# Optimization experiments

Measured on AMD Instinct MI355X. Metric: run time of the kernel, lower is better.

## Reference

```python
import jax, jax.numpy as jnp
import numpy as np
from jax import lax

# fixed perception filters from the paper (ident, sobel_x, sobel_x^T, laplacian)
_IDENT = jnp.array([[0., 0., 0.], [0., 1., 0.], [0., 0., 0.]], dtype=jnp.float32)
_SOBEL_X = jnp.array([[-1., 0., 1.], [-2., 0., 2.], [-1., 0., 1.]], dtype=jnp.float32)
_LAP = jnp.array([[1., 2., 1.], [2., -12., 2.], [1., 2., 1.]], dtype=jnp.float32)
_FILT = jnp.stack([_IDENT, _SOBEL_X, _SOBEL_X.T, _LAP])  # [4,3,3]


def _perceive(x):
    # x: [b, c, h, w] -> [b, 4c, h, w] via circular-pad depthwise 3x3 stencils
    b, c, h, w = x.shape
    y = x.reshape(b * c, 1, h, w)
    y = jnp.pad(y, ((0, 0), (0, 0), (1, 1), (1, 1)), mode='wrap')  # circular pad
    y = lax.conv_general_dilated(y, _FILT[:, None], (1, 1), 'VALID',
                                 dimension_numbers=('NCHW', 'OIHW', 'NCHW'))
    return y.reshape(b, 4 * c, h, w)


def _conv1x1(x, w, b=None):
    # w: [O, C, 1, 1]
    y = jnp.einsum('bchw,oc->bohw', x, w[:, :, 0, 0])
    if b is not None:
        y = y + b[None, :, None, None]
    return y


def _up(z, hw):
    b, c, _, _ = z.shape
    return jax.image.resize(z, (b, c, hw[0], hw[1]), method='bilinear')


def setup_inputs() -> dict:
    key = jax.random.key(0)
    ks = jax.random.split(key, 12)
    D, B = 12, 16
    inp = {
        'x0': jax.random.uniform(ks[0], (B, D, 256, 256), dtype=jnp.float32),
        'x1': jax.random.uniform(ks[1], (B, D, 128, 128), dtype=jnp.float32),
        'x2': jax.random.uniform(ks[2], (B, D, 64, 64), dtype=jnp.float32),
        'w0_1': jax.random.normal(ks[3], (96, 96, 1, 1), dtype=jnp.float32) * 0.05,
        'b0_1': jax.random.normal(ks[4], (96,), dtype=jnp.float32) * 0.05,
        'w0_2': jax.random.normal(ks[5], (D, 96, 1, 1), dtype=jnp.float32) * 0.05,
        'w1_1': jax.random.normal(ks[6], (96, 96, 1, 1), dtype=jnp.float32) * 0.05,
        'b1_1': jax.random.normal(ks[7], (96,), dtype=jnp.float32) * 0.05,
        'w1_2': jax.random.normal(ks[8], (D, 96, 1, 1), dtype=jnp.float32) * 0.05,
        'w2_1': jax.random.normal(ks[9], (96, 48, 1, 1), dtype=jnp.float32) * 0.05,
        'b2_1': jax.random.normal(ks[10], (96,), dtype=jnp.float32) * 0.05,
        'w2_2': jax.random.normal(ks[11], (D, 96, 1, 1), dtype=jnp.float32) * 0.05,
    }
    return inp


def reference(x0, x1, x2, w0_1, b0_1, w0_2, w1_1, b1_1, w1_2, w2_1, b2_1, w2_2):
    z0 = _perceive(x0)  # [B,48,256,256]
    z1 = _perceive(x1)  # [B,48,128,128]
    z2 = _perceive(x2)  # [B,48,64,64]

    # resolution 0: concat with upsampled z1 (to img_size/1)
    h0 = jnp.concatenate([z0, _up(z1, (256, 256))], axis=1)  # [B,96,256,256]
    out0 = _conv1x1(jax.nn.relu(_conv1x1(h0, w0_1, b0_1)), w0_2)

    # resolution 1: concat with upsampled z2 (to img_size/2)
    h1 = jnp.concatenate([z1, _up(z2, (128, 128))], axis=1)  # [B,96,128,128]
    out1 = _conv1x1(jax.nn.relu(_conv1x1(h1, w1_1, b1_1)), w1_2)

    # last resolution: no concat, residual add
    out2 = _conv1x1(jax.nn.relu(_conv1x1(z2, w2_1, b2_1)), w2_2) + x2

    return (out0, out1, out2)
```

## Files before the change

kernel.cpp:

```cpp
#include <hip/hip_runtime.h>


namespace {
constexpr int NB = 16;
constexpr int ND = 12;
}

typedef __attribute__((ext_vector_type(8))) _Float16 f16x8;
typedef __attribute__((ext_vector_type(2))) __fp16  hf16x2;
typedef __attribute__((ext_vector_type(8))) short   s16x8;
typedef __attribute__((ext_vector_type(4))) short   s16x4;
typedef __attribute__((ext_vector_type(4))) float   f32x4;

__device__ __forceinline__ unsigned short f2h(float f) {
    return __builtin_bit_cast(unsigned short, (_Float16)f);
}
__device__ __forceinline__ f16x8 splat8(float x) {
    _Float16 h = (_Float16)x;
    f16x8 v = {h,h,h,h,h,h,h,h};
    return v;
}
__device__ __forceinline__ f16x8 ld8(const unsigned short* p) {
    return __builtin_bit_cast(f16x8, *(const s16x8*)p);
}
__device__ __forceinline__ void st8(unsigned short* p, f16x8 v) {
    *(s16x8*)p = __builtin_bit_cast(s16x8, v);
}

__device__ __forceinline__ void up_taps(int y, int Hc, int& y0, int& y1, float& t1) {
    int j = y >> 1;
    if (y & 1) { y0 = j;            y1 = min(j+1, Hc-1); t1 = 0.25f; }
    else       { y0 = max(j-1, 0);  y1 = j;              t1 = 0.75f; }
}

__device__ __forceinline__ s16x8 repack(f16x8 q0, f16x8 q1, f16x8 q2, f16x8 q3, int j) {
    s16x8 o;
#pragma unroll
    for (int t = 0; t < 8; ++t) {
        int cl = 2*j + (t >> 2);
        _Float16 vv = ((t&3)==0) ? q0[cl] : ((t&3)==1) ? q1[cl]
                    : ((t&3)==2) ? q2[cl] : q3[cl];
        o[t] = (short)__builtin_bit_cast(unsigned short, vv);
    }
    return o;
}

template<int H, int W>
__device__ __forceinline__ void perceive_body(const float* __restrict__ x,
                                              unsigned short* __restrict__ z,
                                              int gid, int tid,
                                              unsigned short* S) {
    constexpr int HW = H*W;
    constexpr int TPX = W/16, BPI = (H/8)*TPX;
    const int b   = gid / BPI;
    const int rem = gid - b*BPI;
    const int tx  = (rem % TPX)*16, ty = (rem / TPX)*8;

#pragma unroll
    for (int i = 0; i < 12; ++i) {
        int e = i*256 + tid;
        if (e < 2880) {
            int c = e / 180, r = e - c*180;
            int ri = r / 18, ci = r - ri*18;
            int gy = (ty - 1 + ri) & (H-1);
            int gx = (tx - 1 + ci) & (W-1);
            unsigned short v = 0;
            if (c < 12) v = f2h(x[(b*ND + c)*HW + gy*W + gx]);
            S[r*16 + c] = v;
        }
    }
    __syncthreads();

    const int p = tid >> 1, h = tid & 1;
    const int py = p >> 4, px = p & 15;
    const unsigned short* Sc = &S[(py*18 + px)*16 + 8*h];
    f16x8 n00=ld8(Sc+0),   n01=ld8(Sc+16),  n02=ld8(Sc+32);
    f16x8 n10=ld8(Sc+288), n11=ld8(Sc+304), n12=ld8(Sc+320);
    f16x8 n20=ld8(Sc+576), n21=ld8(Sc+592), n22=ld8(Sc+608);
    f16x8 two = splat8(2.f), twelve = splat8(12.f);
    f16x8 sx  = (n02-n00) + two*(n12-n10) + (n22-n20);
    f16x8 sy  = (n20-n00) + two*(n21-n01) + (n22-n02);
    f16x8 lap = ((n00+n02)+(n20+n22)) + two*((n01+n10)+(n12+n21)) - twelve*n11;
    unsigned short* zp = z + ((size_t)(b*H + ty+py)*W + tx+px)*48 + 32*h;
    const int nchunk = 4 - 2*h;
#pragma unroll
    for (int j = 0; j < 4; ++j) {
        s16x8 o = repack(n11, sx, sy, lap, j);
        if (j < nchunk) *(s16x8*)(zp + 8*j) = o;
    }
}

__global__ __launch_bounds__(256)
void prep_kernel(const float* __restrict__ x0, const float* __restrict__ x1,
                 const float* __restrict__ x2,
                 const float* __restrict__ w01, const float* __restrict__ w11,
                 const float* __restrict__ w21,
                 const float* __restrict__ w02, const float* __restrict__ w12,
                 const float* __restrict__ w22,
                 unsigned short* __restrict__ x0cl,
                 unsigned short* __restrict__ z1h, unsigned short* __restrict__ z2h,
                 unsigned short* __restrict__ w1f0, unsigned short* __restrict__ w1f1,
                 unsigned short* __restrict__ w1f2,
                 unsigned short* __restrict__ w2h0, unsigned short* __restrict__ w2h1,
                 unsigned short* __restrict__ w2h2)
{
    __shared__ unsigned short S[2880];
    const int tid = threadIdx.x;
    const int bid = blockIdx.x;
    if (bid < 110) {
        int i = bid*256 + tid;
        if (i < 28032) {
            if (i < 9216) {
                int kg = i / 768, rm = i - kg*768, n = rm >> 3, j = rm & 7;
                w1f0[i] = f2h(w01[n*96 + kg*8 + j]);
            } else if (i < 18432) {
                int e = i - 9216;
                int kg = e / 768, rm = e - kg*768, n = rm >> 3, j = rm & 7;
                w1f1[e] = f2h(w11[n*96 + kg*8 + j]);
            } else if (i < 24576) {
                int e = i - 18432;
                int kg = e / 768, rm = e - kg*768, n = rm >> 3, j = rm & 7;
                w1f2[e] = (kg < 6) ? f2h(w21[n*48 + kg*8 + j]) : (unsigned short)0;
            } else {
                int e = i - 24576;
                const float* w = (e < 1152) ? w02 : (e < 2304) ? w12 : w22;
                unsigned short* d = (e < 1152) ? w2h0 : (e < 2304) ? w2h1 : w2h2;
                int q = (e >= 2304) ? e-2304 : (e >= 1152) ? e-1152 : e;
                d[q] = f2h(w[q]);
            }
        }
    } else if (bid < 110 + 4096) {
        int pix = (bid-110)*256 + tid;
        int b = pix >> 16, rem = pix & 65535;
        const float* xp = x0 + (size_t)b*ND*65536 + rem;
        s16x8 r0, r1;
#pragma unroll
        for (int c = 0; c < 8; ++c) r0[c] = (short)f2h(xp[c*65536]);
#pragma unroll
        for (int c = 0; c < 4; ++c) r1[c] = (short)f2h(xp[(8+c)*65536]);
#pragma unroll
        for (int c = 4; c < 8; ++c) r1[c] = 0;
        unsigned short* d = &x0cl[(size_t)pix*16];
        *(s16x8*)d       = r0;
        *(s16x8*)(d + 8) = r1;
    } else if (bid < 110 + 4096 + 2048) {
        perceive_body<128,128>(x1, z1h, bid - (110+4096), tid, S);
    } else {
        perceive_body<64,64>(x2, z2h, bid - (110+4096+2048), tid, S);
    }
}

template<int RES>
__device__ __forceinline__
void res_body(const unsigned short* __restrict__ xcl,
              const unsigned short* __restrict__ zown,
              const unsigned short* __restrict__ zc,
              const float* __restrict__ xres,
              const unsigned short* __restrict__ w1f,
              const float* __restrict__ b1,
              const unsigned short* __restrict__ w2h,
              float* __restrict__ out,
              int bid, int tid, unsigned short* Alds)
{
    constexpr int H  = (RES==0)?256:(RES==1)?128:64;
    constexpr int W  = H, Hc = H/2, Wc = W/2;
    constexpr int HW = H*W;
    constexpr int TPX = W/16, BPI = (H/16)*TPX;
    constexpr int NBLK = NB*BPI;
    constexpr int NK  = (RES==2)?2:3;

    constexpr int cpx = NBLK >> 3;
    const int gid = (bid & 7)*cpx + (bid >> 3);
    const int b   = gid / BPI;
    const int rem = gid - b*BPI;
    const int tx  = (rem % TPX)*16, ty = (rem / TPX)*16;

    const int wid = tid >> 6, lane = tid & 63;
    const int fr  = lane & 15, g = lane >> 4;
    const int r   = tid;
    const int py  = r >> 4, px = r & 15;
    const int gy  = ty + py, gx = tx + px;

    if (RES == 0) {
        int ym=(gy-1)&(H-1), yp=(gy+1)&(H-1);
        int xm=(gx-1)&(W-1), xq=(gx+1)&(W-1);
        const unsigned short* bp = xcl + (size_t)b*HW*16;
        const int r00=(ym*W+xm)*16, r01=(ym*W+gx)*16, r02=(ym*W+xq)*16;
        const int r10=(gy*W+xm)*16, r11=(gy*W+gx)*16, r12=(gy*W+xq)*16;
        const int r20=(yp*W+xm)*16, r21=(yp*W+gx)*16, r22=(yp*W+xq)*16;
#pragma unroll
        for (int grp = 0; grp < 2; ++grp) {
            const int off = grp*8;
            f16x8 n00=ld8(&bp[r00+off]), n01=ld8(&bp[r01+off]), n02=ld8(&bp[r02+off]);
            f16x8 n10=ld8(&bp[r10+off]), n11=ld8(&bp[r11+off]), n12=ld8(&bp[r12+off]);
            f16x8 n20=ld8(&bp[r20+off]), n21=ld8(&bp[r21+off]), n22=ld8(&bp[r22+off]);
            f16x8 two = splat8(2.f), twelve = splat8(12.f);
            f16x8 sx  = (n02-n00) + two*(n12-n10) + (n22-n20);
            f16x8 sy  = (n20-n00) + two*(n21-n01) + (n22-n02);
            f16x8 lap = ((n00+n02)+(n20+n22)) + two*((n01+n10)+(n12+n21)) - twelve*n11;
            const int jn = grp ? 2 : 4;
#pragma unroll
            for (int j = 0; j < 4; ++j) {
                s16x8 o = repack(n11, sx, sy, lap, j);
                if (j < jn) *(s16x8*)&Alds[(grp*4 + j)*2048 + r*8] = o;
            }
        }
    } else {
        const unsigned short* src = &zown[((size_t)(b*H + gy)*W + gx)*48];
#pragma unroll
        for (int j = 0; j < 6; ++j)
            *(s16x8*)&Alds[j*2048 + r*8] = *(const s16x8*)&src[8*j];
        if (RES == 2) {
            s16x8 zz = {0,0,0,0,0,0,0,0};
            *(s16x8*)&Alds[6*2048 + r*8] = zz;
            *(s16x8*)&Alds[7*2048 + r*8] = zz;
        }
    }

    if (RES != 2) {
        int ys0, ys1, xs0, xs1; float tyw, txw;
        up_taps(gy, Hc, ys0, ys1, tyw);
        up_taps(gx, Wc, xs0, xs1, txw);
        float wy0 = 1.f - tyw, wx0 = 1.f - txw;
        f16x8 w00 = splat8(wy0*wx0), w01v = splat8(wy0*txw);
        f16x8 w10 = splat8(tyw*wx0), w11v = splat8(tyw*txw);
        const int o00 = ((b*Hc + ys0)*Wc + xs0)*48;
        const int o01 = ((b*Hc + ys0)*Wc + xs1)*48;
        const int o10 = ((b*Hc + ys1)*Wc + xs0)*48;
        const int o11 = ((b*Hc + ys1)*Wc + xs1)*48;
#pragma unroll
        for (int j = 0; j < 6; ++j) {
            f16x8 t00 = ld8(&zc[o00 + 8*j]);
            f16x8 t01 = ld8(&zc[o01 + 8*j]);
            f16x8 t10 = ld8(&zc[o10 + 8*j]);
            f16x8 t11 = ld8(&zc[o11 + 8*j]);
            f16x8 v = t00*w00 + t01*w01v + t10*w10 + t11*w11v;
            st8(&Alds[(6 + j)*2048 + r*8], v);
        }
    }

    f16x8 w1r[3][6];
#pragma unroll
    for (int ks = 0; ks < NK; ++ks)
#pragma unroll
        for (int nt = 0; nt < 6; ++nt)
            w1r[ks][nt] = ld8(&w1f[((ks*4 + g)*96 + nt*16 + fr)*8]);
    f16x8 w2r[3];
#pragma unroll
    for (int ks = 0; ks < 3; ++ks) {
        s16x8 v = {0,0,0,0,0,0,0,0};
        if (fr < 12) v = *(const s16x8*)&w2h[fr*96 + ks*32 + g*8];
        w2r[ks] = __builtin_bit_cast(f16x8, v);
    }

#pragma unroll 1
    for (int h2 = 0; h2 < 2; ++h2) {
        const int rbase = wid*64 + h2*32;

        f32x4 acc[2][6] = {};
#pragma unroll
        for (int ks = 0; ks < NK; ++ks) {
            const int kgo = (ks*4 + g)*2048;
            f16x8 a0 = ld8(&Alds[kgo + (rbase +      fr)*8]);
            f16x8 a1 = ld8(&Alds[kgo + (rbase + 16 + fr)*8]);
#pragma unroll
            for (int nt = 0; nt < 6; ++nt) {
                acc[0][nt] = __builtin_amdgcn_mfma_f32_16x16x32_f16(w1r[ks][nt], a0, acc[0][nt], 0, 0, 0);
                acc[1][nt] = __builtin_amdgcn_mfma_f32_16x16x32_f16(w1r[ks][nt], a1, acc[1][nt], 0, 0, 0);
            }
        }

#pragma unroll
        for (int nt = 0; nt < 6; ++nt) {
            const float4 bv4 = *(const float4*)&b1[nt*16 + g*4];
#pragma unroll
            for (int pt = 0; pt < 2; ++pt) {
                float h0 = fmaxf(acc[pt][nt][0] + bv4.x, 0.f);
                float h1 = fmaxf(acc[pt][nt][1] + bv4.y, 0.f);
                float h2f_ = fmaxf(acc[pt][nt][2] + bv4.z, 0.f);
                float h3 = fmaxf(acc[pt][nt][3] + bv4.w, 0.f);
                hf16x2 lo = __builtin_amdgcn_cvt_pkrtz(h0, h1);
                hf16x2 hi = __builtin_amdgcn_cvt_pkrtz(h2f_, h3);
                uint2 qq;
                qq.x = __builtin_bit_cast(unsigned int, lo);
                qq.y = __builtin_bit_cast(unsigned int, hi);
                int row = rbase + pt*16 + fr;
                *(s16x4*)&Alds[(nt*2 + (g>>1))*2048 + row*8 + (g&1)*4] =
                    __builtin_bit_cast(s16x4, qq);
            }
        }

        f32x4 acc2[2] = {};
#pragma unroll
        for (int ks = 0; ks < 3; ++ks) {
            const int kgo = (ks*4 + g)*2048;
#pragma unroll
            for (int m = 0; m < 2; ++m) {
                f16x8 ah = ld8(&Alds[kgo + (rbase + m*16 + fr)*8]);
                acc2[m] = __builtin_amdgcn_mfma_f32_16x16x32_f16(ah, w2r[ks], acc2[m], 0, 0, 0);
            }
        }

        if (fr < 12) {
            const int chbase = (b*ND + fr)*HW;
#pragma unroll
            for (int m = 0; m < 2; ++m) {
                int oy = ty + 4*wid + 2*h2 + m;
                int ox = tx + g*4;
                float4 vv;
                vv.x = acc2[m][0]; vv.y = acc2[m][1];
                vv.z = acc2[m][2]; vv.w = acc2[m][3];
                if (RES == 2) {
                    const float4 rr = *(const float4*)&xres[chbase + oy*W + ox];
                    vv.x += rr.x; vv.y += rr.y; vv.z += rr.z; vv.w += rr.w;
                }
                *(float4*)&out[chbase + oy*W + ox] = vv;
            }
        }
    }
}

__global__ __launch_bounds__(256, 3)
void fused_res(const unsigned short* __restrict__ x0cl,
               const unsigned short* __restrict__ z1h,
               const unsigned short* __restrict__ z2h,
               const float* __restrict__ x2,
               const unsigned short* __restrict__ w1f0,
               const unsigned short* __restrict__ w1f1,
               const unsigned short* __restrict__ w1f2,
               const float* __restrict__ b0_1, const float* __restrict__ b1_1,
               const float* __restrict__ b2_1,
               const unsigned short* __restrict__ w2h0,
               const unsigned short* __restrict__ w2h1,
               const unsigned short* __restrict__ w2h2,
               float* __restrict__ out)
{
    __shared__ unsigned short Alds[12*256*8];
    const int tid = threadIdx.x;
    const int bid = blockIdx.x;
    float* out1 = out + NB*ND*256*256;
    float* out2 = out1 + NB*ND*128*128;
    if (bid < 4096) {
        res_body<0>(x0cl, nullptr, z1h, nullptr, w1f0, b0_1, w2h0, out,
                    bid, tid, Alds);
    } else if (bid < 4096 + 1024) {
        res_body<1>(nullptr, z1h, z2h, nullptr, w1f1, b1_1, w2h1, out1,
                    bid - 4096, tid, Alds);
    } else {
        res_body<2>(nullptr, z2h, nullptr, x2, w1f2, b2_1, w2h2, out2,
                    bid - (4096 + 1024), tid, Alds);
    }
}

extern "C" void kernel_launch(void* const* d_in, const int* in_sizes, int n_in,
                              void* d_out, int out_size, void* d_ws, size_t ws_size,
                              hipStream_t stream) {
    const float* x0   = (const float*)d_in[0];
    const float* x1   = (const float*)d_in[1];
    const float* x2   = (const float*)d_in[2];
    const float* w0_1 = (const float*)d_in[3];
    const float* b0_1 = (const float*)d_in[4];
    const float* w0_2 = (const float*)d_in[5];
    const float* w1_1 = (const float*)d_in[6];
    const float* b1_1 = (const float*)d_in[7];
    const float* w1_2 = (const float*)d_in[8];
    const float* w2_1 = (const float*)d_in[9];
    const float* b2_1 = (const float*)d_in[10];
    const float* w2_2 = (const float*)d_in[11];
    float* out = (float*)d_out;

    unsigned short* z1h  = (unsigned short*)d_ws;
    unsigned short* z2h  = z1h + 16*128*128*48;
    unsigned short* w1f0 = z2h + 16*64*64*48;
    unsigned short* w1f1 = w1f0 + 9216;
    unsigned short* w1f2 = w1f1 + 9216;
    unsigned short* w2h0 = w1f2 + 6144;
    unsigned short* w2h1 = w2h0 + 1152;
    unsigned short* w2h2 = w2h1 + 1152;
    unsigned short* x0cl = w2h2 + 1152;

    prep_kernel<<<6766, 256, 0, stream>>>(x0, x1, x2,
                                          w0_1, w1_1, w2_1, w0_2, w1_2, w2_2,
                                          x0cl, z1h, z2h,
                                          w1f0, w1f1, w1f2, w2h0, w2h1, w2h2);

    fused_res<<<4096 + 1024 + 256, 256, 0, stream>>>(
        x0cl, z1h, z2h, x2,
        w1f0, w1f1, w1f2,
        b0_1, b1_1, b2_1,
        w2h0, w2h1, w2h2, out);
}
```

Measured before the change: 91.56 us.

## Reorder perception channels to planar groups, enlarge perceive tiles, reorder block dispatch

The 48 perception channels are stored grouped by filter ([ident x12, sobel_x x12, ...]) instead of interleaved per channel. Packing then becomes cheap vector shuffles rather than per-element scalar repacks, and the first-layer weights are permuted to match. Perceive blocks now cover 16x16 pixels with all 12 channels per thread instead of 8x16 tiles split across thread pairs, which halves the block count and drops the zero-padded channel slots. The fused kernel also schedules the small resolution-2 and resolution-1 blocks before the large resolution-0 ones, which may change tail behaviour.

Result: slower. 97.35 us (+6.3%).

```diff
diff --git a/kernel.cpp b/kernel.cpp
--- a/kernel.cpp
+++ b/kernel.cpp
@@ -26,6 +26,12 @@
 __device__ __forceinline__ void st8(unsigned short* p, f16x8 v) {
     *(s16x8*)p = __builtin_bit_cast(s16x8, v);
 }
+__device__ __forceinline__ s16x8 cat_lo_lo(f16x8 a, f16x8 b) {
+    return __builtin_bit_cast(s16x8, __builtin_shufflevector(a, b, 0,1,2,3, 8,9,10,11));
+}
+__device__ __forceinline__ s16x8 cat_hi_lo(f16x8 a, f16x8 b) {
+    return __builtin_bit_cast(s16x8, __builtin_shufflevector(a, b, 4,5,6,7, 8,9,10,11));
+}
 
 __device__ __forceinline__ void up_taps(int y, int Hc, int& y0, int& y1, float& t1) {
     int j = y >> 1;
@@ -33,17 +39,14 @@
     else       { y0 = max(j-1, 0);  y1 = j;              t1 = 0.75f; }
 }
 
-__device__ __forceinline__ s16x8 repack(f16x8 q0, f16x8 q1, f16x8 q2, f16x8 q3, int j) {
-    s16x8 o;
-#pragma unroll
-    for (int t = 0; t < 8; ++t) {
-        int cl = 2*j + (t >> 2);
-        _Float16 vv = ((t&3)==0) ? q0[cl] : ((t&3)==1) ? q1[cl]
-                    : ((t&3)==2) ? q2[cl] : q3[cl];
-        o[t] = (short)__builtin_bit_cast(unsigned short, vv);
-    }
-    return o;
-}
+#define PACK6(OUT_STMT)                                                     \
+    { s16x8 o;                                                              \
+      o = __builtin_bit_cast(s16x8, n11g0);      { constexpr int j = 0; OUT_STMT } \
+      o = cat_lo_lo(n11g1, sxg0);                { constexpr int j = 1; OUT_STMT } \
+      o = cat_hi_lo(sxg0, sxg1);                 { constexpr int j = 2; OUT_STMT } \
+      o = __builtin_bit_cast(s16x8, syg0);       { constexpr int j = 3; OUT_STMT } \
+      o = cat_lo_lo(syg1, lapg0);                { constexpr int j = 4; OUT_STMT } \
+      o = cat_hi_lo(lapg0, lapg1);               { constexpr int j = 5; OUT_STMT } }
 
 template<int H, int W>
 __device__ __forceinline__ void perceive_body(const float* __restrict__ x,
@@ -51,43 +54,42 @@
                                               int gid, int tid,
                                               unsigned short* S) {
     constexpr int HW = H*W;
-    constexpr int TPX = W/16, BPI = (H/8)*TPX;
+    constexpr int TPX = W/16, BPI = (H/16)*TPX;
     const int b   = gid / BPI;
     const int rem = gid - b*BPI;
-    const int tx  = (rem % TPX)*16, ty = (rem / TPX)*8;
-
-#pragma unroll
-    for (int i = 0; i < 12; ++i) {
+    const int tx  = (rem % TPX)*16, ty = (rem / TPX)*16;
+
+#pragma unroll
+    for (int i = 0; i < 16; ++i) {
         int e = i*256 + tid;
-        if (e < 2880) {
-            int c = e / 180, r = e - c*180;
+        if (e < 3888) {
+            int c = e / 324, r = e - c*324;
             int ri = r / 18, ci = r - ri*18;
             int gy = (ty - 1 + ri) & (H-1);
             int gx = (tx - 1 + ci) & (W-1);
-            unsigned short v = 0;
-            if (c < 12) v = f2h(x[(b*ND + c)*HW + gy*W + gx]);
-            S[r*16 + c] = v;
+            S[(ri*18 + ci)*16 + c] = f2h(x[(b*ND + c)*HW + gy*W + gx]);
         }
     }
     __syncthreads();
 
-    const int p = tid >> 1, h = tid & 1;
-    const int py = p >> 4, px = p & 15;
-    const unsigned short* Sc = &S[(py*18 + px)*16 + 8*h];
-    f16x8 n00=ld8(Sc+0),   n01=ld8(Sc+16),  n02=ld8(Sc+32);
-    f16x8 n10=ld8(Sc+288), n11=ld8(Sc+304), n12=ld8(Sc+320);
-    f16x8 n20=ld8(Sc+576), n21=ld8(Sc+592), n22=ld8(Sc+608);
-    f16x8 two = splat8(2.f), twelve = splat8(12.f);
-    f16x8 sx  = (n02-n00) + two*(n12-n10) + (n22-n20);
-    f16x8 sy  = (n20-n00) + two*(n21-n01) + (n22-n02);
-    f16x8 lap = ((n00+n02)+(n20+n22)) + two*((n01+n10)+(n12+n21)) - twelve*n11;
-    unsigned short* zp = z + ((size_t)(b*H + ty+py)*W + tx+px)*48 + 32*h;
-    const int nchunk = 4 - 2*h;
-#pragma unroll
-    for (int j = 0; j < 4; ++j) {
-        s16x8 o = repack(n11, sx, sy, lap, j);
-        if (j < nchunk) *(s16x8*)(zp + 8*j) = o;
-    }
+    const int py = tid >> 4, px = tid & 15;
+    const unsigned short* Sc = &S[(py*18 + px)*16];
+    f16x8 n11g0, n11g1, sxg0, sxg1, syg0, syg1, lapg0, lapg1;
+#pragma unroll
+    for (int grp = 0; grp < 2; ++grp) {
+        const unsigned short* Sg = Sc + 8*grp;
+        f16x8 n00=ld8(Sg+0),   n01=ld8(Sg+16),  n02=ld8(Sg+32);
+        f16x8 n10=ld8(Sg+288), n11=ld8(Sg+304), n12=ld8(Sg+320);
+        f16x8 n20=ld8(Sg+576), n21=ld8(Sg+592), n22=ld8(Sg+608);
+        f16x8 two = splat8(2.f), twelve = splat8(12.f);
+        f16x8 sx  = (n02-n00) + two*(n12-n10) + (n22-n20);
+        f16x8 sy  = (n20-n00) + two*(n21-n01) + (n22-n02);
+        f16x8 lap = ((n00+n02)+(n20+n22)) + two*((n01+n10)+(n12+n21)) - twelve*n11;
+        if (grp == 0) { n11g0=n11; sxg0=sx; syg0=sy; lapg0=lap; }
+        else          { n11g1=n11; sxg1=sx; syg1=sy; lapg1=lap; }
+    }
+    unsigned short* zp = z + ((size_t)(b*H + ty+py)*W + tx+px)*48;
+    PACK6( *(s16x8*)(zp + 8*j) = o; )
 }
 
 __global__ __launch_bounds__(256)
@@ -104,23 +106,32 @@
                  unsigned short* __restrict__ w2h0, unsigned short* __restrict__ w2h1,
                  unsigned short* __restrict__ w2h2)
 {
-    __shared__ unsigned short S[2880];
+    __shared__ unsigned short S[18*18*16];
     const int tid = threadIdx.x;
     const int bid = blockIdx.x;
     if (bid < 110) {
         int i = bid*256 + tid;
         if (i < 28032) {
-            if (i < 9216) {
-                int kg = i / 768, rm = i - kg*768, n = rm >> 3, j = rm & 7;
-                w1f0[i] = f2h(w01[n*96 + kg*8 + j]);
-            } else if (i < 18432) {
-                int e = i - 9216;
-                int kg = e / 768, rm = e - kg*768, n = rm >> 3, j = rm & 7;
-                w1f1[e] = f2h(w11[n*96 + kg*8 + j]);
+            if (i < 18432) {
+                const float* w = (i < 9216) ? w01 : w11;
+                unsigned short* d = (i < 9216) ? w1f0 : w1f1;
+                int e = (i < 9216) ? i : i - 9216;
+                int kg = e / 768, rm = e - kg*768, n = rm >> 3, jj = rm & 7;
+                int kh = kg*8 + jj;
+                int orig;
+                if (kh < 48) { int f = kh/12, c = kh-12*f; orig = 4*c + f; }
+                else { int q = kh-48; int f = q/12, c = q-12*f; orig = 48 + 4*c + f; }
+                d[e] = f2h(w[n*96 + orig]);
             } else if (i < 24576) {
                 int e = i - 18432;
-                int kg = e / 768, rm = e - kg*768, n = rm >> 3, j = rm & 7;
-                w1f2[e] = (kg < 6) ? f2h(w21[n*48 + kg*8 + j]) : (unsigned short)0;
+                int kg = e / 768, rm = e - kg*768, n = rm >> 3, jj = rm & 7;
+                int kh = kg*8 + jj;
+                unsigned short v = 0;
+                if (kh < 48) {
+                    int f = kh/12, c = kh-12*f;
+                    v = f2h(w21[n*48 + 4*c + f]);
+                }
+                w1f2[e] = v;
             } else {
                 int e = i - 24576;
                 const float* w = (e < 1152) ? w02 : (e < 2304) ? w12 : w22;
@@ -143,10 +154,10 @@
         unsigned short* d = &x0cl[(size_t)pix*16];
         *(s16x8*)d       = r0;
         *(s16x8*)(d + 8) = r1;
-    } else if (bid < 110 + 4096 + 2048) {
+    } else if (bid < 110 + 4096 + 1024) {
         perceive_body<128,128>(x1, z1h, bid - (110+4096), tid, S);
     } else {
-        perceive_body<64,64>(x2, z2h, bid - (110+4096+2048), tid, S);
+        perceive_body<64,64>(x2, z2h, bid - (110+4096+1024), tid, S);
     }
 }
 
@@ -188,6 +199,7 @@
         const int r00=(ym*W+xm)*16, r01=(ym*W+gx)*16, r02=(ym*W+xq)*16;
         const int r10=(gy*W+xm)*16, r11=(gy*W+gx)*16, r12=(gy*W+xq)*16;
         const int r20=(yp*W+xm)*16, r21=(yp*W+gx)*16, r22=(yp*W+xq)*16;
+        f16x8 n11g0, n11g1, sxg0, sxg1, syg0, syg1, lapg0, lapg1;
 #pragma unroll
         for (int grp = 0; grp < 2; ++grp) {
             const int off = grp*8;
@@ -198,13 +210,10 @@
             f16x8 sx  = (n02-n00) + two*(n12-n10) + (n22-n20);
             f16x8 sy  = (n20-n00) + two*(n21-n01) + (n22-n02);
             f16x8 lap = ((n00+n02)+(n20+n22)) + two*((n01+n10)+(n12+n21)) - twelve*n11;
-            const int jn = grp ? 2 : 4;
-#pragma unroll
-            for (int j = 0; j < 4; ++j) {
-                s16x8 o = repack(n11, sx, sy, lap, j);
-                if (j < jn) *(s16x8*)&Alds[(grp*4 + j)*2048 + r*8] = o;
-            }
-        }
+            if (grp == 0) { n11g0=n11; sxg0=sx; syg0=sy; lapg0=lap; }
+            else          { n11g1=n11; sxg1=sx; syg1=sy; lapg1=lap; }
+        }
+        PACK6( *(s16x8*)&Alds[j*2048 + r*8] = o; )
     } else {
         const unsigned short* src = &zown[((size_t)(b*H + gy)*W + gx)*48];
 #pragma unroll
@@ -340,15 +349,15 @@
     const int bid = blockIdx.x;
     float* out1 = out + NB*ND*256*256;
     float* out2 = out1 + NB*ND*128*128;
-    if (bid < 4096) {
+    if (bid < 256) {
+        res_body<2>(nullptr, z2h, nullptr, x2, w1f2, b2_1, w2h2, out2,
+                    bid, tid, Alds);
+    } else if (bid < 256 + 1024) {
+        res_body<1>(nullptr, z1h, z2h, nullptr, w1f1, b1_1, w2h1, out1,
+                    bid - 256, tid, Alds);
+    } else {
         res_body<0>(x0cl, nullptr, z1h, nullptr, w1f0, b0_1, w2h0, out,
-                    bid, tid, Alds);
-    } else if (bid < 4096 + 1024) {
-        res_body<1>(nullptr, z1h, z2h, nullptr, w1f1, b1_1, w2h1, out1,
-                    bid - 4096, tid, Alds);
-    } else {
-        res_body<2>(nullptr, z2h, nullptr, x2, w1f2, b2_1, w2h2, out2,
-                    bid - (4096 + 1024), tid, Alds);
+                    bid - 1280, tid, Alds);
     }
 }
 
@@ -379,12 +388,13 @@
     unsigned short* w2h2 = w2h1 + 1152;
     unsigned short* x0cl = w2h2 + 1152;
 
-    prep_kernel<<<6766, 256, 0, stream>>>(x0, x1, x2,
-                                          w0_1, w1_1, w2_1, w0_2, w1_2, w2_2,
-                                          x0cl, z1h, z2h,
-                                          w1f0, w1f1, w1f2, w2h0, w2h1, w2h2);
-
-    fused_res<<<4096 + 1024 + 256, 256, 0, stream>>>(
+    prep_kernel<<<110 + 4096 + 1024 + 256, 256, 0, stream>>>(
+        x0, x1, x2,
+        w0_1, w1_1, w2_1, w0_2, w1_2, w2_2,
+        x0cl, z1h, z2h,
+        w1f0, w1f1, w1f2, w2h0, w2h1, w2h2);
+
+    fused_res<<<256 + 1024 + 4096, 256, 0, stream>>>(
         x0cl, z1h, z2h, x2,
         w1f0, w1f1, w1f2,
         b0_1, b1_1, b2_1,
```
